# Kernel optimization log

Measured on AMD Instinct MI355X. Metric: run time of the kernel, lower is better.

## Reference

```python
import jax, jax.numpy as jnp
import numpy as np

B, T, C, H = 2, 2048, 1024, 16
D = C // H
EPS = 1e-5
ROPE_BASE = 10000.0


def _rope_tables(t, d, base=ROPE_BASE):
    half = d // 2
    inv_freq = 1.0 / (base ** (jnp.arange(half, dtype=jnp.float32) / half))
    freqs = jnp.arange(t, dtype=jnp.float32)[:, None] * inv_freq[None, :]  # [T, D/2]
    emb = jnp.concatenate([freqs, freqs], axis=-1)  # [T, D]
    return jnp.cos(emb), jnp.sin(emb)


def _rotate_half(x):
    a, b = jnp.split(x, 2, axis=-1)
    return jnp.concatenate([-b, a], axis=-1)


def setup_inputs() -> dict:
    key = jax.random.key(0)
    k0, k1, k2 = jax.random.split(key, 3)
    s = 0.02  # typical init scale
    return {
        "x": jax.random.normal(k0, (B, T, C), jnp.float32),
        "attention_mask": jnp.ones((B, T), jnp.int32),
        "w_qkv": jax.random.normal(k1, (3 * C, C), jnp.float32) * s,
        "b_qkv": jnp.zeros((3 * C,), jnp.float32),
        "w_o": jax.random.normal(k2, (C, C), jnp.float32) * s,
        "b_o": jnp.zeros((C,), jnp.float32),
        "rms_w": jnp.ones((C,), jnp.float32),
    }


def reference(x, attention_mask, w_qkv, b_qkv, w_o, b_o, rms_w):
    b, t, c = x.shape
    h = H
    d = c // h
    # RMSNorm
    xn = x * jax.lax.rsqrt(jnp.mean(x * x, axis=-1, keepdims=True) + EPS) * rms_w
    # fused QKV projection -> [B, T, 3, H, D]
    qkv = (jnp.einsum('btc,oc->bto', xn, w_qkv) + b_qkv).reshape(b, t, 3, h, d)
    q, k, v = qkv[:, :, 0], qkv[:, :, 1], qkv[:, :, 2]
    # RoPE (position_ids = arange(T))
    cos, sin = _rope_tables(t, d)
    cos = cos[None, :, None, :]  # [1, T, 1, D]
    sin = sin[None, :, None, :]
    q = q * cos + _rotate_half(q) * sin
    k = k * cos + _rotate_half(k) * sin
    # causal attention (flash_attn_func semantics: scale 1/sqrt(d), causal)
    scores = jnp.einsum('bqhd,bkhd->bhqk', q, k) / jnp.sqrt(jnp.float32(d))
    causal = jnp.tril(jnp.ones((t, t), dtype=bool))
    scores = jnp.where(causal[None, None], scores, jnp.float32(-1e30))
    attn = jax.nn.softmax(scores, axis=-1)
    out = jnp.einsum('bhqk,bkhd->bqhd', attn, v).reshape(b, t, c)
    return jnp.einsum('btc,oc->bto', out, w_o) + b_o
```

## Files before the change

kernel.cpp:

```cpp
#include <hip/hip_runtime.h>
#include <math.h>

constexpr int Bb = 2;
constexpr int Tt = 2048;
constexpr int Cc = 1024;
constexpr int Hh = 16;
constexpr int M_ROWS = Bb * Tt;
constexpr float EPSV = 1e-5f;

typedef __attribute__((ext_vector_type(4))) float f32x4;
typedef __attribute__((ext_vector_type(8))) __bf16 bf16x8;
using u16 = unsigned short;

union Frag8 {
    u16 u[8];
    unsigned int ui[4];
    uint4 v;
    bf16x8 b;
};

__device__ __forceinline__ u16 f2bf(float f) {
    union { float f; unsigned int u; } c;
    c.f = f;
    unsigned int r = (c.u + 0x7fffu + ((c.u >> 16) & 1u)) >> 16;
    return (u16)r;
}
__device__ __forceinline__ float bf2f(u16 u) {
    union { unsigned int i; float f; } c;
    c.i = ((unsigned int)u) << 16;
    return c.f;
}

__device__ __forceinline__ void gload_lds16(const void* g, void* l) {
    __builtin_amdgcn_global_load_lds(
        (__attribute__((address_space(1))) void*)const_cast<void*>(g),
        (__attribute__((address_space(3))) void*)l, 16, 0, 0);
}

__global__ __launch_bounds__(256) void prep_k(const float* __restrict__ w_qkv,
                                              u16* __restrict__ wqkv_bf,
                                              const float* __restrict__ w_o,
                                              u16* __restrict__ wo_bf,
                                              float* __restrict__ cosT,
                                              float* __restrict__ sinT,
                                              const float* __restrict__ x,
                                              const float* __restrict__ rms_w,
                                              u16* __restrict__ xn) {
    __shared__ float ws_[4];
    int blk = blockIdx.x;
    int tid = threadIdx.x;
    if (blk < 3072) {
        int i = (blk * 256 + tid) * 4;
        float4 v = *(const float4*)&w_qkv[i];
        ushort4 o;
        o.x = f2bf(v.x); o.y = f2bf(v.y); o.z = f2bf(v.z); o.w = f2bf(v.w);
        *(ushort4*)&wqkv_bf[i] = o;
    } else if (blk < 4096) {
        int i = ((blk - 3072) * 256 + tid) * 4;
        float4 v = *(const float4*)&w_o[i];
        ushort4 o;
        o.x = f2bf(v.x); o.y = f2bf(v.y); o.z = f2bf(v.z); o.w = f2bf(v.w);
        *(ushort4*)&wo_bf[i] = o;
    } else if (blk < 4352) {
        int lin = (blk - 4096) * 256 + tid;
        int tt = lin >> 5, j = lin & 31;
        float inv = exp2f(-(float)j * (log2f(10000.0f) / 32.0f));
        float a = (float)tt * inv;
        cosT[lin] = cosf(a);
        sinT[lin] = sinf(a);
    } else {
        int row = blk - 4352;
        const float* xr = x + (size_t)row * Cc;
        float4 v = *(const float4*)&xr[tid * 4];
        float ss = v.x * v.x + v.y * v.y + v.z * v.z + v.w * v.w;
        #pragma unroll
        for (int off = 32; off > 0; off >>= 1) ss += __shfl_down(ss, off);
        if ((tid & 63) == 0) ws_[tid >> 6] = ss;
        __syncthreads();
        float tot = ws_[0] + ws_[1] + ws_[2] + ws_[3];
        float r = rsqrtf(tot * (1.0f / (float)Cc) + EPSV);
        float4 wv = *(const float4*)&rms_w[tid * 4];
        ushort4 o;
        o.x = f2bf(v.x * r * wv.x);
        o.y = f2bf(v.y * r * wv.y);
        o.z = f2bf(v.z * r * wv.z);
        o.w = f2bf(v.w * r * wv.w);
        *(ushort4*)&xn[(size_t)row * Cc + tid * 4] = o;
    }
}

template<bool BF16OUT>
__global__ __launch_bounds__(256) void gemm_mfma_k(const u16* __restrict__ A,
                                                   const u16* __restrict__ W,
                                                   const float* __restrict__ bias,
                                                   void* __restrict__ Ov,
                                                   int M, int N, int K) {
    __shared__ __align__(16) u16 As[128 * 64];
    __shared__ __align__(16) u16 Bs[64 * 64];

    const int tid = threadIdx.x;
    const int w = tid >> 6;
    const int l = tid & 63;
    const int wr = w >> 1;
    const int wc = w & 1;
    const int q = l & 15;
    const int g = l >> 4;

    const int m0 = blockIdx.y * 128;
    const int n0 = blockIdx.x * 64;

    const int srow = l >> 3;
    const int cph = l & 7;
    const int cl = cph ^ srow;

    f32x4 acc[4][2];
    #pragma unroll
    for (int i = 0; i < 4; ++i)
        #pragma unroll
        for (int j = 0; j < 2; ++j)
            acc[i][j] = (f32x4){0.f, 0.f, 0.f, 0.f};

    const int nkt = K >> 6;
    for (int kt = 0; kt < nkt; ++kt) {
        const int k0 = kt << 6;
        __syncthreads();
        #pragma unroll
        for (int iss = 0; iss < 4; ++iss) {
            int r = w * 32 + iss * 8 + srow;
            gload_lds16(A + (size_t)(m0 + r) * K + k0 + cl * 8,
                        &As[(w * 32 + iss * 8) * 64]);
        }
        #pragma unroll
        for (int iss = 0; iss < 2; ++iss) {
            int r = w * 16 + iss * 8 + srow;
            gload_lds16(W + (size_t)(n0 + r) * K + k0 + cl * 8,
                        &Bs[(w * 16 + iss * 8) * 64]);
        }
        __syncthreads();

        #pragma unroll
        for (int kk = 0; kk < 2; ++kk) {
            Frag8 af[4], bf[2];
            const int ca = kk * 4 + g;
            #pragma unroll
            for (int i = 0; i < 4; ++i) {
                int ra = wr * 64 + i * 16 + q;
                af[i] = *(const Frag8*)&As[ra * 64 + ((ca ^ (ra & 7)) * 8)];
            }
            #pragma unroll
            for (int j = 0; j < 2; ++j) {
                int rb = wc * 32 + j * 16 + q;
                bf[j] = *(const Frag8*)&Bs[rb * 64 + ((ca ^ (rb & 7)) * 8)];
            }
            #pragma unroll
            for (int i = 0; i < 4; ++i)
                #pragma unroll
                for (int j = 0; j < 2; ++j)
                    acc[i][j] = __builtin_amdgcn_mfma_f32_16x16x32_bf16(
                        af[i].b, bf[j].b, acc[i][j], 0, 0, 0);
        }
    }

    #pragma unroll
    for (int i = 0; i < 4; ++i) {
        int row = m0 + wr * 64 + i * 16 + g * 4;
        #pragma unroll
        for (int j = 0; j < 2; ++j) {
            int col = n0 + wc * 32 + j * 16 + q;
            float bb = bias[col];
            #pragma unroll
            for (int r2 = 0; r2 < 4; ++r2) {
                float val = acc[i][j][r2] + bb;
                if (BF16OUT)
                    ((u16*)Ov)[(size_t)(row + r2) * N + col] = f2bf(val);
                else
                    ((float*)Ov)[(size_t)(row + r2) * N + col] = val;
            }
        }
    }
}

__global__ __launch_bounds__(256) void rope_pack_k(const u16* __restrict__ qkv,
                                                   const float* __restrict__ cosT,
                                                   const float* __restrict__ sinT,
                                                   u16* __restrict__ Qb,
                                                   u16* __restrict__ KL,
                                                   u16* __restrict__ VL) {
    const int jt = blockIdx.x;
    const int t0 = jt * 64;
    const int h = blockIdx.y, b = blockIdx.z;
    const int t = threadIdx.x;
    const int bh = b * Hh + h;
    __shared__ u16 Vs[64 * 64];
    constexpr float QSC = 0.125f * 1.44269504089f;
    const size_t tilebase = ((size_t)bh * 32 + jt) * 4096;

    {
        int row = t >> 2, d16 = (t & 3) * 16;
        const u16* vp = qkv + (size_t)(b * Tt + t0 + row) * 3072 + 2048 + h * 64 + d16;
        *(uint4*)&Vs[row * 64 + d16]     = *(const uint4*)vp;
        *(uint4*)&Vs[row * 64 + d16 + 8] = *(const uint4*)(vp + 8);
    }

    {
        int row = t >> 2, d0 = (t & 3) * 8;
        int g = row >> 4, q15 = row & 15, g2 = t & 3;
        size_t rb = (size_t)(b * Tt + t0 + row) * 3072 + h * 64;
        const u16* qp = qkv + rb;
        const u16* kp = qkv + rb + 1024;
        Frag8 qlo, qhi, klo, khi;
        qlo.v = *(const uint4*)&qp[d0];
        qhi.v = *(const uint4*)&qp[d0 + 32];
        klo.v = *(const uint4*)&kp[d0];
        khi.v = *(const uint4*)&kp[d0 + 32];
        const float* cp = &cosT[(t0 + row) * 32 + d0];
        const float* sp = &sinT[(t0 + row) * 32 + d0];
        float4 c0 = *(const float4*)cp, c1 = *(const float4*)(cp + 4);
        float4 s0 = *(const float4*)sp, s1 = *(const float4*)(sp + 4);
        float cc[8] = {c0.x, c0.y, c0.z, c0.w, c1.x, c1.y, c1.z, c1.w};
        float ss[8] = {s0.x, s0.y, s0.z, s0.w, s1.x, s1.y, s1.z, s1.w};
        Frag8 oql, oqh, okl, okh;
        #pragma unroll
        for (int i = 0; i < 8; ++i) {
            float ql = bf2f(qlo.u[i]), qh = bf2f(qhi.u[i]);
            float kl = bf2f(klo.u[i]), kh = bf2f(khi.u[i]);
            oql.u[i] = f2bf((ql * cc[i] - qh * ss[i]) * QSC);
            oqh.u[i] = f2bf((qh * cc[i] + ql * ss[i]) * QSC);
            okl.u[i] = f2bf(kl * cc[i] - kh * ss[i]);
            okh.u[i] = f2bf(kh * cc[i] + kl * ss[i]);
        }
        u16* qd = Qb + ((size_t)bh * Tt + t0 + row) * 64;
        *(uint4*)&qd[d0]      = oql.v;
        *(uint4*)&qd[d0 + 32] = oqh.v;
        *(uint4*)&KL[tilebase + (size_t)(0 * 4 + g) * 512 + (g2 * 16 + q15) * 8] = okl.v;
        *(uint4*)&KL[tilebase + (size_t)(1 * 4 + g) * 512 + (g2 * 16 + q15) * 8] = okh.v;
    }
    __syncthreads();

    {
        int d = t >> 2, kq = (t & 3) * 16;
        int dg = d >> 4, q15v = d & 15;
        int kkv = (t & 3) >> 1;
        int g2a = ((t & 3) & 1) * 2;
        Frag8 a, b2;
        #pragma unroll
        for (int j = 0; j < 16; ++j) {
            int slot = kq + j;
            int key = ((slot >> 5) * 2 + ((slot >> 2) & 1)) * 16
                    + ((slot >> 3) & 3) * 4 + (slot & 3);
            u16 vv = Vs[key * 64 + d];
            if (j < 8) a.u[j] = vv; else b2.u[j - 8] = vv;
        }
        u16* base = VL + tilebase + (size_t)(kkv * 4 + dg) * 512;
        *(uint4*)&base[(g2a * 16 + q15v) * 8]       = a.v;
        *(uint4*)&base[((g2a + 1) * 16 + q15v) * 8] = b2.v;
    }
}

__global__ __launch_bounds__(256, 4) void attn_mfma_k(const u16* __restrict__ Qb,
                                                      const u16* __restrict__ KL,
                                                      const u16* __restrict__ VL,
                                                      u16* __restrict__ out) {
    const int i = blockIdx.x;
    int c, bh;
    if (i < 512) { c = 31 - (i >> 5); bh = i & 31; }
    else         { int k = i - 512; c = k >> 5; bh = k & 31; }
    const int b = bh >> 4, h = bh & 15;

    const int t = threadIdx.x;
    const int w4 = t >> 6;
    const int l = t & 63;
    const int q15 = l & 15;
    const int g2 = l >> 4;

    Frag8 qf[2];
    {
        int qrow = c * 64 + w4 * 16 + q15;
        const u16* qp = Qb + ((size_t)bh * Tt + qrow) * 64;
        qf[0] = *(const Frag8*)&qp[g2 * 8];
        qf[1] = *(const Frag8*)&qp[32 + g2 * 8];
    }

    Frag8 ones;
    #pragma unroll
    for (int e = 0; e < 8; ++e) ones.u[e] = 0x3F80;

    f32x4 acco[4];
    #pragma unroll
    for (int dg = 0; dg < 4; ++dg) acco[dg] = (f32x4){0.f, 0.f, 0.f, 0.f};
    f32x4 acc_l = (f32x4){0.f, 0.f, 0.f, 0.f};

    const u16* kp0 = KL + ((size_t)bh * 32) * 4096 + l * 8;
    const u16* kp1 = kp0 + 2048;
    const u16* vp0 = VL + ((size_t)bh * 32) * 4096 + l * 8;
    const u16* vp1 = vp0 + 2048;

    for (int j = 0; j <= c; ++j) {
        Frag8 kf[2][4];
        #pragma unroll
        for (int g = 0; g < 4; ++g) {
            kf[0][g] = *(const Frag8*)&kp0[g * 512];
            kf[1][g] = *(const Frag8*)&kp1[g * 512];
        }
        f32x4 sacc[4];
        __builtin_amdgcn_s_setprio(1);
        #pragma unroll
        for (int g = 0; g < 4; ++g) {
            sacc[g] = (f32x4){0.f, 0.f, 0.f, 0.f};
            sacc[g] = __builtin_amdgcn_mfma_f32_16x16x32_bf16(
                kf[0][g].b, qf[0].b, sacc[g], 0, 0, 0);
            sacc[g] = __builtin_amdgcn_mfma_f32_16x16x32_bf16(
                kf[1][g].b, qf[1].b, sacc[g], 0, 0, 0);
        }
        __builtin_amdgcn_s_setprio(0);

        Frag8 vf[2][4];
        #pragma unroll
        for (int dg = 0; dg < 4; ++dg) {
            vf[0][dg] = *(const Frag8*)&vp0[dg * 512];
            vf[1][dg] = *(const Frag8*)&vp1[dg * 512];
        }

        if (j == c) {
            #pragma unroll
            for (int g = 0; g < 4; ++g)
                #pragma unroll
                for (int r = 0; r < 4; ++r)
                    if (g * 16 + g2 * 4 + r > w4 * 16 + q15) sacc[g][r] = -1e30f;
        }

        Frag8 pa[2];
        #pragma unroll
        for (int kk = 0; kk < 2; ++kk)
            #pragma unroll
            for (int e = 0; e < 8; ++e)
                pa[kk].b[e] = (__bf16)exp2f(sacc[2 * kk + (e >> 2)][e & 3]);

        __builtin_amdgcn_s_setprio(1);
        acc_l = __builtin_amdgcn_mfma_f32_16x16x32_bf16(pa[0].b, ones.b, acc_l, 0, 0, 0);
        acc_l = __builtin_amdgcn_mfma_f32_16x16x32_bf16(pa[1].b, ones.b, acc_l, 0, 0, 0);
        #pragma unroll
        for (int dg = 0; dg < 4; ++dg) {
            acco[dg] = __builtin_amdgcn_mfma_f32_16x16x32_bf16(
                pa[0].b, vf[0][dg].b, acco[dg], 0, 0, 0);
            acco[dg] = __builtin_amdgcn_mfma_f32_16x16x32_bf16(
                pa[1].b, vf[1][dg].b, acco[dg], 0, 0, 0);
        }
        __builtin_amdgcn_s_setprio(0);

        kp0 += 4096; kp1 += 4096;
        vp0 += 4096; vp1 += 4096;
    }

    float lr[4];
    #pragma unroll
    for (int r = 0; r < 4; ++r) lr[r] = 1.f / acc_l[r];
    const int qbase = c * 64 + w4 * 16;
    #pragma unroll
    for (int dg = 0; dg < 4; ++dg)
        #pragma unroll
        for (int r = 0; r < 4; ++r)
            out[((size_t)(b * Tt + qbase + g2 * 4 + r)) * Cc + h * 64 + dg * 16 + q15] =
                f2bf(acco[dg][r] * lr[r]);
}

extern "C" void kernel_launch(void* const* d_in, const int* in_sizes, int n_in,
                              void* d_out, int out_size, void* d_ws, size_t ws_size,
                              hipStream_t stream) {
    const float* x      = (const float*)d_in[0];
    const float* w_qkv  = (const float*)d_in[2];
    const float* b_qkv  = (const float*)d_in[3];
    const float* w_o    = (const float*)d_in[4];
    const float* b_o    = (const float*)d_in[5];
    const float* rms_w  = (const float*)d_in[6];
    float* out = (float*)d_out;

    char* ws = (char*)d_ws;
    u16*   xn_bf   = (u16*)ws;
    u16*   KL      = (u16*)(ws + (size_t)(8 << 20));
    u16*   VL      = (u16*)(ws + (size_t)(16 << 20));
    u16*   Qb      = (u16*)(ws + (size_t)(24 << 20));
    u16*   qkvb    = (u16*)(ws + (size_t)(32 << 20));
    u16*   wqkv_bf = (u16*)(ws + (size_t)(56 << 20));
    u16*   wo_bf   = (u16*)(ws + (size_t)(62 << 20));
    float* cosT    = (float*)(ws + (size_t)(64 << 20));
    float* sinT    = (float*)(ws + (size_t)(64 << 20) + (1 << 18));
    u16*   attn_bf = xn_bf;

    prep_k<<<dim3(8448), dim3(256), 0, stream>>>(w_qkv, wqkv_bf, w_o, wo_bf,
                                                 cosT, sinT, x, rms_w, xn_bf);
    gemm_mfma_k<true><<<dim3(3 * Cc / 64, M_ROWS / 128), dim3(256), 0, stream>>>(
        xn_bf, wqkv_bf, b_qkv, qkvb, M_ROWS, 3 * Cc, Cc);
    rope_pack_k<<<dim3(Tt / 64, Hh, Bb), dim3(256), 0, stream>>>(
        qkvb, cosT, sinT, Qb, KL, VL);
    attn_mfma_k<<<dim3(1024), dim3(256), 0, stream>>>(Qb, KL, VL, attn_bf);
    gemm_mfma_k<false><<<dim3(Cc / 64, M_ROWS / 128), dim3(256), 0, stream>>>(
        attn_bf, wo_bf, b_o, out, M_ROWS, Cc, Cc);
}
```

Measured before the change: 114.2 us.

## Process two query chunks per attention block to reuse K/V fragments

Each attention block now handles 128 query rows (two 64-row chunks) instead of 64, sharing every K and V fragment load between both chunks. The grid halves and launch bounds drop to 2 blocks per CU to allow the doubled accumulator state. This halves K/V global traffic per query, but costs extra registers, lower occupancy, and one redundant score tile per block for the first chunk.

```diff
diff --git a/kernel.cpp b/kernel.cpp
--- a/kernel.cpp
+++ b/kernel.cpp
@@ -257,14 +257,14 @@
     }
 }
 
-__global__ __launch_bounds__(256, 4) void attn_mfma_k(const u16* __restrict__ Qb,
+__global__ __launch_bounds__(256, 2) void attn_mfma_k(const u16* __restrict__ Qb,
                                                       const u16* __restrict__ KL,
                                                       const u16* __restrict__ VL,
                                                       u16* __restrict__ out) {
     const int i = blockIdx.x;
     int c, bh;
-    if (i < 512) { c = 31 - (i >> 5); bh = i & 31; }
-    else         { int k = i - 512; c = k >> 5; bh = k & 31; }
+    if (i < 256) { c = 15 - (i >> 5); bh = i & 31; }
+    else         { int k = i - 256; c = k >> 5; bh = k & 31; }
     const int b = bh >> 4, h = bh & 15;
 
     const int t = threadIdx.x;
@@ -273,44 +273,60 @@
     const int q15 = l & 15;
     const int g2 = l >> 4;
 
-    Frag8 qf[2];
-    {
-        int qrow = c * 64 + w4 * 16 + q15;
-        const u16* qp = Qb + ((size_t)bh * Tt + qrow) * 64;
-        qf[0] = *(const Frag8*)&qp[g2 * 8];
-        qf[1] = *(const Frag8*)&qp[32 + g2 * 8];
+    Frag8 qfA[2], qfB[2];
+    {
+        int qrowA = c * 128 + w4 * 16 + q15;
+        const u16* qpA = Qb + ((size_t)bh * Tt + qrowA) * 64;
+        qfA[0] = *(const Frag8*)&qpA[g2 * 8];
+        qfA[1] = *(const Frag8*)&qpA[32 + g2 * 8];
+        const u16* qpB = qpA + (size_t)64 * 64;
+        qfB[0] = *(const Frag8*)&qpB[g2 * 8];
+        qfB[1] = *(const Frag8*)&qpB[32 + g2 * 8];
     }
 
     Frag8 ones;
     #pragma unroll
     for (int e = 0; e < 8; ++e) ones.u[e] = 0x3F80;
 
-    f32x4 acco[4];
+    f32x4 accoA[4], accoB[4];
     #pragma unroll
-    for (int dg = 0; dg < 4; ++dg) acco[dg] = (f32x4){0.f, 0.f, 0.f, 0.f};
-    f32x4 acc_l = (f32x4){0.f, 0.f, 0.f, 0.f};
+    for (int dg = 0; dg < 4; ++dg) {
+        accoA[dg] = (f32x4){0.f, 0.f, 0.f, 0.f};
+        accoB[dg] = (f32x4){0.f, 0.f, 0.f, 0.f};
+    }
+    f32x4 acc_lA = (f32x4){0.f, 0.f, 0.f, 0.f};
+    f32x4 acc_lB = (f32x4){0.f, 0.f, 0.f, 0.f};
 
     const u16* kp0 = KL + ((size_t)bh * 32) * 4096 + l * 8;
     const u16* kp1 = kp0 + 2048;
     const u16* vp0 = VL + ((size_t)bh * 32) * 4096 + l * 8;
     const u16* vp1 = vp0 + 2048;
 
-    for (int j = 0; j <= c; ++j) {
+    const int jdA = 2 * c;
+    const int jmax = 2 * c + 1;
+
+    for (int j = 0; j <= jmax; ++j) {
         Frag8 kf[2][4];
         #pragma unroll
         for (int g = 0; g < 4; ++g) {
             kf[0][g] = *(const Frag8*)&kp0[g * 512];
             kf[1][g] = *(const Frag8*)&kp1[g * 512];
         }
-        f32x4 sacc[4];
+
+        f32x4 saccA[4], saccB[4];
         __builtin_amdgcn_s_setprio(1);
         #pragma unroll
         for (int g = 0; g < 4; ++g) {
-            sacc[g] = (f32x4){0.f, 0.f, 0.f, 0.f};
-            sacc[g] = __builtin_amdgcn_mfma_f32_16x16x32_bf16(
-                kf[0][g].b, qf[0].b, sacc[g], 0, 0, 0);
-            sacc[g] = __builtin_amdgcn_mfma_f32_16x16x32_bf16(
-                kf[1][g].b, qf[1].b, sacc[g], 0, 0, 0);
+            saccA[g] = (f32x4){0.f, 0.f, 0.f, 0.f};
+            saccA[g] = __builtin_amdgcn_mfma_f32_16x16x32_bf16(
+                kf[0][g].b, qfA[0].b, saccA[g], 0, 0, 0);
+            saccA[g] = __builtin_amdgcn_mfma_f32_16x16x32_bf16(
+                kf[1][g].b, qfA[1].b, saccA[g], 0, 0, 0);
+            saccB[g] = (f32x4){0.f, 0.f, 0.f, 0.f};
+            saccB[g] = __builtin_amdgcn_mfma_f32_16x16x32_bf16(
+                kf[0][g].b, qfB[0].b, saccB[g], 0, 0, 0);
+            saccB[g] = __builtin_amdgcn_mfma_f32_16x16x32_bf16(
+                kf[1][g].b, qfB[1].b, saccB[g], 0, 0, 0);
         }
         __builtin_amdgcn_s_setprio(0);
 
@@ -321,47 +337,89 @@
             vf[1][dg] = *(const Frag8*)&vp1[dg * 512];
         }
 
-        if (j == c) {
+        if (j == jdA) {
             #pragma unroll
             for (int g = 0; g < 4; ++g)
                 #pragma unroll
                 for (int r = 0; r < 4; ++r)
-                    if (g * 16 + g2 * 4 + r > w4 * 16 + q15) sacc[g][r] = -1e30f;
-        }
-
-        Frag8 pa[2];
-        #pragma unroll
-        for (int kk = 0; kk < 2; ++kk)
-            #pragma unroll
-            for (int e = 0; e < 8; ++e)
-                pa[kk].b[e] = (__bf16)exp2f(sacc[2 * kk + (e >> 2)][e & 3]);
-
-        __builtin_amdgcn_s_setprio(1);
-        acc_l = __builtin_amdgcn_mfma_f32_16x16x32_bf16(pa[0].b, ones.b, acc_l, 0, 0, 0);
-        acc_l = __builtin_amdgcn_mfma_f32_16x16x32_bf16(pa[1].b, ones.b, acc_l, 0, 0, 0);
-        #pragma unroll
-        for (int dg = 0; dg < 4; ++dg) {
-            acco[dg] = __builtin_amdgcn_mfma_f32_16x16x32_bf16(
-                pa[0].b, vf[0][dg].b, acco[dg], 0, 0, 0);
-            acco[dg] = __builtin_amdgcn_mfma_f32_16x16x32_bf16(
-                pa[1].b, vf[1][dg].b, acco[dg], 0, 0, 0);
-        }
-        __builtin_amdgcn_s_setprio(0);
+                    if (g * 16 + g2 * 4 + r > w4 * 16 + q15) saccA[g][r] = -1e30f;
+        }
+        if (j == jmax) {
+            #pragma unroll
+            for (int g = 0; g < 4; ++g)
+                #pragma unroll
+                for (int r = 0; r < 4; ++r)
+                    if (g * 16 + g2 * 4 + r > w4 * 16 + q15) saccB[g][r] = -1e30f;
+        }
+
+        if (j <= jdA) {
+            Frag8 pa[2];
+            #pragma unroll
+            for (int kk = 0; kk < 2; ++kk)
+                #pragma unroll
+                for (int e = 0; e < 8; ++e)
+                    pa[kk].b[e] = (__bf16)exp2f(saccA[2 * kk + (e >> 2)][e & 3]);
+            __builtin_amdgcn_s_setprio(1);
+            acc_lA = __builtin_amdgcn_mfma_f32_16x16x32_bf16(pa[0].b, ones.b, acc_lA, 0, 0, 0);
+            acc_lA = __builtin_amdgcn_mfma_f32_16x16x32_bf16(pa[1].b, ones.b, acc_lA, 0, 0, 0);
+            #pragma unroll
+            for (int dg = 0; dg < 4; ++dg) {
+                accoA[dg] = __builtin_amdgcn_mfma_f32_16x16x32_bf16(
+                    pa[0].b, vf[0][dg].b, accoA[dg], 0, 0, 0);
+                accoA[dg] = __builtin_amdgcn_mfma_f32_16x16x32_bf16(
+                    pa[1].b, vf[1][dg].b, accoA[dg], 0, 0, 0);
+            }
+            __builtin_amdgcn_s_setprio(0);
+        }
+
+        {
+            Frag8 pb[2];
+            #pragma unroll
+            for (int kk = 0; kk < 2; ++kk)
+                #pragma unroll
+                for (int e = 0; e < 8; ++e)
+                    pb[kk].b[e] = (__bf16)exp2f(saccB[2 * kk + (e >> 2)][e & 3]);
+            __builtin_amdgcn_s_setprio(1);
+            acc_lB = __builtin_amdgcn_mfma_f32_16x16x32_bf16(pb[0].b, ones.b, acc_lB, 0, 0, 0);
+            acc_lB = __builtin_amdgcn_mfma_f32_16x16x32_bf16(pb[1].b, ones.b, acc_lB, 0, 0, 0);
+            #pragma unroll
+            for (int dg = 0; dg < 4; ++dg) {
+                accoB[dg] = __builtin_amdgcn_mfma_f32_16x16x32_bf16(
+                    pb[0].b, vf[0][dg].b, accoB[dg], 0, 0, 0);
+                accoB[dg] = __builtin_amdgcn_mfma_f32_16x16x32_bf16(
+                    pb[1].b, vf[1][dg].b, accoB[dg], 0, 0, 0);
+            }
+            __builtin_amdgcn_s_setprio(0);
+        }
 
         kp0 += 4096; kp1 += 4096;
         vp0 += 4096; vp1 += 4096;
     }
 
-    float lr[4];
-    #pragma unroll
-    for (int r = 0; r < 4; ++r) lr[r] = 1.f / acc_l[r];
-    const int qbase = c * 64 + w4 * 16;
-    #pragma unroll
-    for (int dg = 0; dg < 4; ++dg)
-        #pragma unroll
-        for (int r = 0; r < 4; ++r)
-            out[((size_t)(b * Tt + qbase + g2 * 4 + r)) * Cc + h * 64 + dg * 16 + q15] =
-                f2bf(acco[dg][r] * lr[r]);
+    {
+        float lr[4];
+        #pragma unroll
+        for (int r = 0; r < 4; ++r) lr[r] = 1.f / acc_lA[r];
+        const int qbase = c * 128 + w4 * 16;
+        #pragma unroll
+        for (int dg = 0; dg < 4; ++dg)
+            #pragma unroll
+            for (int r = 0; r < 4; ++r)
+                out[((size_t)(b * Tt + qbase + g2 * 4 + r)) * Cc + h * 64 + dg * 16 + q15] =
+                    f2bf(accoA[dg][r] * lr[r]);
+    }
+    {
+        float lr[4];
+        #pragma unroll
+        for (int r = 0; r < 4; ++r) lr[r] = 1.f / acc_lB[r];
+        const int qbase = c * 128 + 64 + w4 * 16;
+        #pragma unroll
+        for (int dg = 0; dg < 4; ++dg)
+            #pragma unroll
+            for (int r = 0; r < 4; ++r)
+                out[((size_t)(b * Tt + qbase + g2 * 4 + r)) * Cc + h * 64 + dg * 16 + q15] =
+                    f2bf(accoB[dg][r] * lr[r]);
+    }
 }
 
 extern "C" void kernel_launch(void* const* d_in, const int* in_sizes, int n_in,
@@ -393,7 +451,7 @@
         xn_bf, wqkv_bf, b_qkv, qkvb, M_ROWS, 3 * Cc, Cc);
     rope_pack_k<<<dim3(Tt / 64, Hh, Bb), dim3(256), 0, stream>>>(
         qkvb, cosT, sinT, Qb, KL, VL);
-    attn_mfma_k<<<dim3(1024), dim3(256), 0, stream>>>(Qb, KL, VL, attn_bf);
+    attn_mfma_k<<<dim3(512), dim3(256), 0, stream>>>(Qb, KL, VL, attn_bf);
     gemm_mfma_k<false><<<dim3(Cc / 64, M_ROWS / 128), dim3(256), 0, stream>>>(
         attn_bf, wo_bf, b_o, out, M_ROWS, Cc, Cc);
 }
```

Result: no change. 116.0 us (+1.6%).
